# Kernel tuning notes

Hardware: AMD Instinct MI355X
Metric: run time of the kernel (lower is better)

Reference implementation:

```python
import jax, jax.numpy as jnp
import numpy as np

B, H, S, D = 2, 16, 2048, 64
NUM_BUCKETS = 32
MAX_DISTANCE = 256


def setup_inputs() -> dict:
    key = jax.random.key(0)
    kq, kk, kv, kb, kl = jax.random.split(key, 5)
    q = jax.random.normal(kq, (B, H, S, D), dtype=jnp.float32)
    k = jax.random.normal(kk, (B, H, S, D), dtype=jnp.float32)
    v = jax.random.normal(kv, (B, H, S, D), dtype=jnp.float32)
    bias_table = jax.random.normal(kb, (NUM_BUCKETS, H), dtype=jnp.float32)
    event_length = jax.random.randint(kl, (B,), 1, S + 1, dtype=jnp.int64)
    return {"q": q, "k": k, "v": v, "bias_table": bias_table, "event_length": event_length}


def _relative_position_bucket(relative_position):
    # T5-style bucketing exactly as the torch module: n = -rel_pos
    half = NUM_BUCKETS // 2  # 16
    n = -relative_position
    is_small = n < half
    # guard log for the branch not taken (n<=0); where() masks it out
    nf = jnp.maximum(n, 1).astype(jnp.float32)
    val_if_large = half + jnp.minimum(
        jnp.log(nf / half) / np.log(MAX_DISTANCE / half) * (NUM_BUCKETS - half),
        NUM_BUCKETS - 1 - half,
    ).astype(jnp.int32)
    ret = jnp.where(is_small, n, val_if_large)
    return jnp.clip(ret, 0, NUM_BUCKETS - 1)


def _compute_bias(bias_table, seq_len):
    ctx = jnp.arange(seq_len)[:, None]
    mem = jnp.arange(seq_len)[None, :]
    rp_bucket = _relative_position_bucket(mem - ctx)  # (S,S)
    values = bias_table[rp_bucket]                    # (S,S,H)
    return jnp.transpose(values, (2, 0, 1))[None]     # (1,H,S,S)


def reference(q, k, v, bias_table, event_length):
    seq_len = q.shape[2]
    head_dim = q.shape[3]
    # scaled QK^T: (B,H,S,S)
    logits = jnp.einsum("bhsd,bhtd->bhst", q, k) / np.sqrt(head_dim).astype(np.float32)
    logits = logits + _compute_bias(bias_table, seq_len)
    # key-side padding mask from per-event lengths
    mask = jnp.arange(seq_len)[None, None, None, :] < event_length[:, None, None, None]
    logits = jnp.where(mask, logits, jnp.float32(-1e9))
    attn = jax.nn.softmax(logits, axis=-1)
    # dropout p=0.01 omitted (eval-mode deterministic reference)
    return jnp.einsum("bhst,bhtd->bhsd", attn, v)
```

## Files before the change

### kernel.cpp

```cpp
#include <hip/hip_runtime.h>
#include <hip/hip_bf16.h>

#define B_ 2
#define H_ 16
#define S_ 2048
#define D_ 64
#define BQ 128
#define BK 64
#define LDSTR 72
#define LOG2E 1.4426950408889634f
#define FIXM 10.0f

#if __has_builtin(__builtin_amdgcn_exp2f)
#define EXP2F(x) __builtin_amdgcn_exp2f(x)
#else
#define EXP2F(x) __expf((x) * 0.6931471805599453f)
#endif

typedef _Float16 half8 __attribute__((ext_vector_type(8)));
typedef float floatx4 __attribute__((ext_vector_type(4)));

__global__ __launch_bounds__(256, 2)
void t5_attn_kernel(const float* __restrict__ qg_, const float* __restrict__ kg_,
                    const float* __restrict__ vg_, const float* __restrict__ bt,
                    const int* __restrict__ elen, float* __restrict__ outg_)
{
    __shared__ __align__(16) _Float16 Kl[BK][LDSTR];
    __shared__ __align__(16) _Float16 Vt[D_][LDSTR];
    __shared__ __align__(16) _Float16 Pl[4][32][LDSTR];
    __shared__ float lut[256];

    const int qblk = blockIdx.x;
    const int h    = blockIdx.y;
    const int b    = blockIdx.z;
    const int tid  = threadIdx.x;
    const int wave = tid >> 6;
    const int lane = tid & 63;
    const int quad = lane >> 4;
    const int t16  = lane & 15;

    {
        int n = tid;
        int bucket;
        if (n < 16) {
            bucket = n;
        } else {
            int vl = (int)(__log2f((float)n * 0.0625f) * 4.0f);
            bucket = 16 + (vl < 15 ? vl : 15);
        }
        lut[n] = bt[bucket * H_ + h] * LOG2E - FIXM;
    }
    const float sh_next = FIXM - bt[h] * LOG2E;
    const float sh_far  = FIXM - bt[31 * H_ + h] * LOG2E;

    const int len = (elen[1] == 0) ? elen[2 * b] : elen[b];
    const int ntiles = (len + BK - 1) >> 6;

    const size_t bh = ((size_t)b * H_ + h) * (size_t)(S_ * D_);
    const float* qg = qg_ + bh;
    const float* kg = kg_ + bh;
    const float* vg = vg_ + bh;
    float*       og = outg_ + bh;

    half8 qf[2][2];
    #pragma unroll
    for (int rg = 0; rg < 2; ++rg) {
        const float qscale = 0.125f * LOG2E;
        const int row = qblk * BQ + wave * 32 + rg * 16 + t16;
        const float* qp = qg + (size_t)row * D_ + quad * 8;
        #pragma unroll
        for (int c = 0; c < 2; ++c) {
            const float4* p = reinterpret_cast<const float4*>(qp + c * 32);
            float4 x0 = p[0], x1 = p[1];
            half8 hv;
            hv[0] = (_Float16)(x0.x * qscale); hv[1] = (_Float16)(x0.y * qscale);
            hv[2] = (_Float16)(x0.z * qscale); hv[3] = (_Float16)(x0.w * qscale);
            hv[4] = (_Float16)(x1.x * qscale); hv[5] = (_Float16)(x1.y * qscale);
            hv[6] = (_Float16)(x1.z * qscale); hv[7] = (_Float16)(x1.w * qscale);
            qf[rg][c] = hv;
        }
    }

    floatx4 zero4 = {0.f, 0.f, 0.f, 0.f};
    floatx4 acc[2][4];
    float l_[2][4];
    #pragma unroll
    for (int rg = 0; rg < 2; ++rg) {
        #pragma unroll
        for (int nb = 0; nb < 4; ++nb) acc[rg][nb] = zero4;
        #pragma unroll
        for (int r = 0; r < 4; ++r) l_[rg][r] = 0.f;
    }

    const int i_lo = qblk * BQ + wave * 32;

    float4 kx[2][2];
    float  vx[16];
    auto prefetch = [&](int kt) {
        #pragma unroll
        for (int it = 0; it < 2; ++it) {
            int idx = tid + it * 256;
            int row = idx >> 3;
            int c8  = (idx & 7) << 3;
            const float4* p = reinterpret_cast<const float4*>(
                kg + ((size_t)(kt * BK + row) * D_ + c8));
            kx[it][0] = p[0];
            kx[it][1] = p[1];
        }
        #pragma unroll
        for (int it = 0; it < 2; ++it) {
            int key8 = kt * BK + wave * 8 + it * 32;
            #pragma unroll
            for (int jj = 0; jj < 8; ++jj)
                vx[it * 8 + jj] = vg[(size_t)(key8 + jj) * D_ + lane];
        }
    };

    prefetch(0);

    for (int kt = 0; kt < ntiles; ++kt) {
        __syncthreads();

        #pragma unroll
        for (int it = 0; it < 2; ++it) {
            int idx = tid + it * 256;
            int row = idx >> 3;
            int c8  = (idx & 7) << 3;
            float4 x0 = kx[it][0], x1 = kx[it][1];
            half8 hv;
            hv[0]=(_Float16)x0.x; hv[1]=(_Float16)x0.y; hv[2]=(_Float16)x0.z; hv[3]=(_Float16)x0.w;
            hv[4]=(_Float16)x1.x; hv[5]=(_Float16)x1.y; hv[6]=(_Float16)x1.z; hv[7]=(_Float16)x1.w;
            *reinterpret_cast<half8*>(&Kl[row][c8]) = hv;
        }
        #pragma unroll
        for (int it = 0; it < 2; ++it) {
            int key8 = wave * 8 + it * 32;
            half8 hv;
            #pragma unroll
            for (int jj = 0; jj < 8; ++jj) hv[jj] = (_Float16)vx[it * 8 + jj];
            *reinterpret_cast<half8*>(&Vt[lane][key8]) = hv;
        }
        __syncthreads();

        if (kt + 1 < ntiles) prefetch(kt + 1);

        floatx4 sa[2][4];
        #pragma unroll
        for (int rg = 0; rg < 2; ++rg)
            #pragma unroll
            for (int nb = 0; nb < 4; ++nb) sa[rg][nb] = zero4;
        #pragma unroll
        for (int kc = 0; kc < 2; ++kc) {
            half8 a0 = qf[0][kc], a1 = qf[1][kc];
            #pragma unroll
            for (int nb = 0; nb < 4; ++nb) {
                half8 bb = *reinterpret_cast<const half8*>(
                    &Kl[nb * 16 + t16][kc * 32 + quad * 8]);
                sa[0][nb] = __builtin_amdgcn_mfma_f32_16x16x32_f16(a0, bb, sa[0][nb], 0, 0, 0);
                sa[1][nb] = __builtin_amdgcn_mfma_f32_16x16x32_f16(a1, bb, sa[1][nb], 0, 0, 0);
            }
        }

        const int base = kt * BK;
        if (i_lo + 31 <= base) {
            #pragma unroll
            for (int rg = 0; rg < 2; ++rg)
                #pragma unroll
                for (int nb = 0; nb < 4; ++nb)
                    #pragma unroll
                    for (int r = 0; r < 4; ++r) sa[rg][nb][r] -= sh_next;
        } else if (i_lo >= base + 279) {
            #pragma unroll
            for (int rg = 0; rg < 2; ++rg)
                #pragma unroll
                for (int nb = 0; nb < 4; ++nb)
                    #pragma unroll
                    for (int r = 0; r < 4; ++r) sa[rg][nb][r] -= sh_far;
        } else {
            #pragma unroll
            for (int rg = 0; rg < 2; ++rg) {
                const int d0 = i_lo + rg * 16 + quad * 4 - base - t16;
                #pragma unroll
                for (int nb = 0; nb < 4; ++nb) {
                    #pragma unroll
                    for (int r = 0; r < 4; ++r) {
                        int d = d0 + r - nb * 16;
                        d = d < 0 ? 0 : (d > 255 ? 255 : d);
                        sa[rg][nb][r] += lut[d];
                    }
                }
            }
        }
        if ((kt == ntiles - 1) && (len & 63)) {
            #pragma unroll
            for (int nb = 0; nb < 4; ++nb) {
                bool valid = (base + nb * 16 + t16) < len;
                #pragma unroll
                for (int rg = 0; rg < 2; ++rg)
                    #pragma unroll
                    for (int r = 0; r < 4; ++r)
                        sa[rg][nb][r] = valid ? sa[rg][nb][r] : -1e30f;
            }
        }

        #pragma unroll
        for (int rg = 0; rg < 2; ++rg) {
            #pragma unroll
            for (int nb = 0; nb < 4; ++nb)
                #pragma unroll
                for (int r = 0; r < 4; ++r)
                    sa[rg][nb][r] = EXP2F(sa[rg][nb][r]);
            #pragma unroll
            for (int r = 0; r < 4; ++r)
                l_[rg][r] += (sa[rg][0][r] + sa[rg][1][r]) + (sa[rg][2][r] + sa[rg][3][r]);
        }

        #pragma unroll
        for (int rg = 0; rg < 2; ++rg)
            #pragma unroll
            for (int r = 0; r < 4; ++r)
                #pragma unroll
                for (int nb = 0; nb < 4; ++nb)
                    Pl[wave][rg * 16 + quad * 4 + r][nb * 16 + t16] = (_Float16)sa[rg][nb][r];
        asm volatile("s_waitcnt lgkmcnt(0)" ::: "memory");

        #pragma unroll
        for (int kc = 0; kc < 2; ++kc) {
            half8 a0 = *reinterpret_cast<const half8*>(
                &Pl[wave][t16][kc * 32 + quad * 8]);
            half8 a1 = *reinterpret_cast<const half8*>(
                &Pl[wave][16 + t16][kc * 32 + quad * 8]);
            #pragma unroll
            for (int nb = 0; nb < 4; ++nb) {
                half8 bb = *reinterpret_cast<const half8*>(
                    &Vt[nb * 16 + t16][kc * 32 + quad * 8]);
                acc[0][nb] = __builtin_amdgcn_mfma_f32_16x16x32_f16(a0, bb, acc[0][nb], 0, 0, 0);
                acc[1][nb] = __builtin_amdgcn_mfma_f32_16x16x32_f16(a1, bb, acc[1][nb], 0, 0, 0);
            }
        }
    }

    #pragma unroll
    for (int rg = 0; rg < 2; ++rg) {
        #pragma unroll
        for (int r = 0; r < 4; ++r) {
            float lv = l_[rg][r];
            #pragma unroll
            for (int off = 1; off < 16; off <<= 1)
                lv += __shfl_xor(lv, off, 64);
            float inv = 1.f / lv;
            const int row = qblk * BQ + wave * 32 + rg * 16 + quad * 4 + r;
            #pragma unroll
            for (int nb = 0; nb < 4; ++nb)
                og[(size_t)row * D_ + nb * 16 + t16] = acc[rg][nb][r] * inv;
        }
    }
}

extern "C" void kernel_launch(void* const* d_in, const int* in_sizes, int n_in,
                              void* d_out, int out_size, void* d_ws, size_t ws_size,
                              hipStream_t stream) {
    const float* q  = (const float*)d_in[0];
    const float* k  = (const float*)d_in[1];
    const float* v  = (const float*)d_in[2];
    const float* bt = (const float*)d_in[3];
    const int*   el = (const int*)d_in[4];
    float* out = (float*)d_out;
    dim3 grid(S_ / BQ, H_, B_);
    t5_attn_kernel<<<grid, 256, 0, stream>>>(q, k, v, bt, el, out);
}
```

Baseline: 122.2 us.

## Double-buffer K/V LDS tiles and transpose QK^T MFMA to vectorize P stores

K and V shared-memory tiles become double-buffered, so the next tile is staged after the PV MFMAs and each iteration needs one barrier instead of two. The QK^T MFMA operands are swapped so each lane holds a query row. This lets the P tile be written with packed half4 stores via cvt_pkrtz, and the row sums become one scalar per lane with fewer shuffles. The cost is twice the K/V LDS footprint, which may reduce occupancy, plus changed bias and mask index math.

Result: faster. 117.6 us (-3.8%).

```diff
diff --git a/kernel.cpp b/kernel.cpp
--- a/kernel.cpp
+++ b/kernel.cpp
@@ -18,6 +18,8 @@
 #endif
 
 typedef _Float16 half8 __attribute__((ext_vector_type(8)));
+typedef _Float16 half4 __attribute__((ext_vector_type(4)));
+typedef __fp16   fp16x2 __attribute__((ext_vector_type(2)));
 typedef float floatx4 __attribute__((ext_vector_type(4)));
 
 __global__ __launch_bounds__(256, 2)
@@ -25,8 +27,8 @@
                     const float* __restrict__ vg_, const float* __restrict__ bt,
                     const int* __restrict__ elen, float* __restrict__ outg_)
 {
-    __shared__ __align__(16) _Float16 Kl[BK][LDSTR];
-    __shared__ __align__(16) _Float16 Vt[D_][LDSTR];
+    __shared__ __align__(16) _Float16 Kl[2][BK][LDSTR];
+    __shared__ __align__(16) _Float16 Vt[2][D_][LDSTR];
     __shared__ __align__(16) _Float16 Pl[4][32][LDSTR];
     __shared__ float lut[256];
 
@@ -83,13 +85,12 @@
 
     floatx4 zero4 = {0.f, 0.f, 0.f, 0.f};
     floatx4 acc[2][4];
-    float l_[2][4];
+    float l_[2];
     #pragma unroll
     for (int rg = 0; rg < 2; ++rg) {
         #pragma unroll
         for (int nb = 0; nb < 4; ++nb) acc[rg][nb] = zero4;
-        #pragma unroll
-        for (int r = 0; r < 4; ++r) l_[rg][r] = 0.f;
+        l_[rg] = 0.f;
     }
 
     const int i_lo = qblk * BQ + wave * 32;
@@ -115,12 +116,7 @@
                 vx[it * 8 + jj] = vg[(size_t)(key8 + jj) * D_ + lane];
         }
     };
-
-    prefetch(0);
-
-    for (int kt = 0; kt < ntiles; ++kt) {
-        __syncthreads();
-
+    auto stage = [&](int buf) {
         #pragma unroll
         for (int it = 0; it < 2; ++it) {
             int idx = tid + it * 256;
@@ -130,7 +126,7 @@
             half8 hv;
             hv[0]=(_Float16)x0.x; hv[1]=(_Float16)x0.y; hv[2]=(_Float16)x0.z; hv[3]=(_Float16)x0.w;
             hv[4]=(_Float16)x1.x; hv[5]=(_Float16)x1.y; hv[6]=(_Float16)x1.z; hv[7]=(_Float16)x1.w;
-            *reinterpret_cast<half8*>(&Kl[row][c8]) = hv;
+            *reinterpret_cast<half8*>(&Kl[buf][row][c8]) = hv;
         }
         #pragma unroll
         for (int it = 0; it < 2; ++it) {
@@ -138,11 +134,18 @@
             half8 hv;
             #pragma unroll
             for (int jj = 0; jj < 8; ++jj) hv[jj] = (_Float16)vx[it * 8 + jj];
-            *reinterpret_cast<half8*>(&Vt[lane][key8]) = hv;
-        }
-        __syncthreads();
-
-        if (kt + 1 < ntiles) prefetch(kt + 1);
+            *reinterpret_cast<half8*>(&Vt[buf][lane][key8]) = hv;
+        }
+    };
+
+    prefetch(0);
+    stage(0);
+    __syncthreads();
+
+    for (int kt = 0; kt < ntiles; ++kt) {
+        const int cur = kt & 1;
+        const bool more = (kt + 1) < ntiles;
+        if (more) prefetch(kt + 1);
 
         floatx4 sa[2][4];
         #pragma unroll
@@ -151,13 +154,12 @@
             for (int nb = 0; nb < 4; ++nb) sa[rg][nb] = zero4;
         #pragma unroll
         for (int kc = 0; kc < 2; ++kc) {
-            half8 a0 = qf[0][kc], a1 = qf[1][kc];
-            #pragma unroll
-            for (int nb = 0; nb < 4; ++nb) {
-                half8 bb = *reinterpret_cast<const half8*>(
-                    &Kl[nb * 16 + t16][kc * 32 + quad * 8]);
-                sa[0][nb] = __builtin_amdgcn_mfma_f32_16x16x32_f16(a0, bb, sa[0][nb], 0, 0, 0);
-                sa[1][nb] = __builtin_amdgcn_mfma_f32_16x16x32_f16(a1, bb, sa[1][nb], 0, 0, 0);
+            #pragma unroll
+            for (int nb = 0; nb < 4; ++nb) {
+                half8 af = *reinterpret_cast<const half8*>(
+                    &Kl[cur][nb * 16 + t16][kc * 32 + quad * 8]);
+                sa[0][nb] = __builtin_amdgcn_mfma_f32_16x16x32_f16(af, qf[0][kc], sa[0][nb], 0, 0, 0);
+                sa[1][nb] = __builtin_amdgcn_mfma_f32_16x16x32_f16(af, qf[1][kc], sa[1][nb], 0, 0, 0);
             }
         }
 
@@ -179,12 +181,12 @@
         } else {
             #pragma unroll
             for (int rg = 0; rg < 2; ++rg) {
-                const int d0 = i_lo + rg * 16 + quad * 4 - base - t16;
+                const int d0 = i_lo + rg * 16 + t16 - base - quad * 4;
                 #pragma unroll
                 for (int nb = 0; nb < 4; ++nb) {
                     #pragma unroll
                     for (int r = 0; r < 4; ++r) {
-                        int d = d0 + r - nb * 16;
+                        int d = d0 - nb * 16 - r;
                         d = d < 0 ? 0 : (d > 255 ? 255 : d);
                         sa[rg][nb][r] += lut[d];
                     }
@@ -194,34 +196,42 @@
         if ((kt == ntiles - 1) && (len & 63)) {
             #pragma unroll
             for (int nb = 0; nb < 4; ++nb) {
-                bool valid = (base + nb * 16 + t16) < len;
-                #pragma unroll
-                for (int rg = 0; rg < 2; ++rg)
-                    #pragma unroll
-                    for (int r = 0; r < 4; ++r)
+                #pragma unroll
+                for (int r = 0; r < 4; ++r) {
+                    bool valid = (base + nb * 16 + quad * 4 + r) < len;
+                    #pragma unroll
+                    for (int rg = 0; rg < 2; ++rg)
                         sa[rg][nb][r] = valid ? sa[rg][nb][r] : -1e30f;
+                }
             }
         }
 
         #pragma unroll
         for (int rg = 0; rg < 2; ++rg) {
+            float s = 0.f;
             #pragma unroll
             for (int nb = 0; nb < 4; ++nb)
                 #pragma unroll
-                for (int r = 0; r < 4; ++r)
+                for (int r = 0; r < 4; ++r) {
                     sa[rg][nb][r] = EXP2F(sa[rg][nb][r]);
-            #pragma unroll
-            for (int r = 0; r < 4; ++r)
-                l_[rg][r] += (sa[rg][0][r] + sa[rg][1][r]) + (sa[rg][2][r] + sa[rg][3][r]);
-        }
-
-        #pragma unroll
-        for (int rg = 0; rg < 2; ++rg)
-            #pragma unroll
-            for (int r = 0; r < 4; ++r)
-                #pragma unroll
-                for (int nb = 0; nb < 4; ++nb)
-                    Pl[wave][rg * 16 + quad * 4 + r][nb * 16 + t16] = (_Float16)sa[rg][nb][r];
+                    s += sa[rg][nb][r];
+                }
+            l_[rg] += s;
+        }
+
+        #pragma unroll
+        for (int rg = 0; rg < 2; ++rg) {
+            #pragma unroll
+            for (int nb = 0; nb < 4; ++nb) {
+                fp16x2 lo = __builtin_amdgcn_cvt_pkrtz(sa[rg][nb][0], sa[rg][nb][1]);
+                fp16x2 hi = __builtin_amdgcn_cvt_pkrtz(sa[rg][nb][2], sa[rg][nb][3]);
+                half4 w;
+                w[0] = (_Float16)lo[0]; w[1] = (_Float16)lo[1];
+                w[2] = (_Float16)hi[0]; w[3] = (_Float16)hi[1];
+                *reinterpret_cast<half4*>(
+                    &Pl[wave][rg * 16 + t16][nb * 16 + quad * 4]) = w;
+            }
+        }
         asm volatile("s_waitcnt lgkmcnt(0)" ::: "memory");
 
         #pragma unroll
@@ -232,27 +242,31 @@
                 &Pl[wave][16 + t16][kc * 32 + quad * 8]);
             #pragma unroll
             for (int nb = 0; nb < 4; ++nb) {
-                half8 bb = *reinterpret_cast<const half8*>(
-                    &Vt[nb * 16 + t16][kc * 32 + quad * 8]);
-                acc[0][nb] = __builtin_amdgcn_mfma_f32_16x16x32_f16(a0, bb, acc[0][nb], 0, 0, 0);
-                acc[1][nb] = __builtin_amdgcn_mfma_f32_16x16x32_f16(a1, bb, acc[1][nb], 0, 0, 0);
-            }
-        }
+                half8 bv = *reinterpret_cast<const half8*>(
+                    &Vt[cur][nb * 16 + t16][kc * 32 + quad * 8]);
+                acc[0][nb] = __builtin_amdgcn_mfma_f32_16x16x32_f16(a0, bv, acc[0][nb], 0, 0, 0);
+                acc[1][nb] = __builtin_amdgcn_mfma_f32_16x16x32_f16(a1, bv, acc[1][nb], 0, 0, 0);
+            }
+        }
+
+        if (more) stage(cur ^ 1);
+        __syncthreads();
     }
 
     #pragma unroll
     for (int rg = 0; rg < 2; ++rg) {
+        float lv = l_[rg];
+        lv += __shfl_xor(lv, 16, 64);
+        lv += __shfl_xor(lv, 32, 64);
+        float inv = 1.f / lv;
         #pragma unroll
         for (int r = 0; r < 4; ++r) {
-            float lv = l_[rg][r];
-            #pragma unroll
-            for (int off = 1; off < 16; off <<= 1)
-                lv += __shfl_xor(lv, off, 64);
-            float inv = 1.f / lv;
-            const int row = qblk * BQ + wave * 32 + rg * 16 + quad * 4 + r;
+            int rowloc = quad * 4 + r;
+            float invr = __shfl(inv, (lane & 48) | rowloc, 64);
+            const int row = qblk * BQ + wave * 32 + rg * 16 + rowloc;
             #pragma unroll
             for (int nb = 0; nb < 4; ++nb)
-                og[(size_t)row * D_ + nb * 16 + t16] = acc[rg][nb][r] * inv;
+                og[(size_t)row * D_ + nb * 16 + t16] = acc[rg][nb][r] * invr;
         }
     }
 }
```
